# Performance work log

Hardware: AMD Instinct MI355X
Metric: run time of the kernel (lower is better)

Reference implementation:

```python
import jax, jax.numpy as jnp
import numpy as np

B, S, H = 2, 4096, 2048
NH, NKV, D = 16, 4, 128
BS, LOCAL, GLOB, STRIDE = 64, 8, 4, 16
SEL = GLOB + LOCAL
SCALE = D ** -0.5
NEG = -1e9


def rotate_half(x):
    x1, x2 = x[..., : D // 2], x[..., D // 2 :]
    return jnp.concatenate([-x2, x1], axis=-1)


def setup_inputs():
    key = jax.random.key(0)
    ks = jax.random.split(key, 5)
    hidden_states = jax.random.normal(ks[0], (B, S, H), dtype=jnp.float32)
    # standard RoPE tables, shape [B, S, D] as the module expects (cos.unsqueeze(1))
    pos = jnp.arange(S, dtype=jnp.float32)
    inv = 1.0 / (10000.0 ** (jnp.arange(0, D, 2, dtype=jnp.float32) / D))
    freqs = pos[:, None] * inv[None, :]
    emb = jnp.concatenate([freqs, freqs], axis=-1)
    cos = jnp.broadcast_to(jnp.cos(emb)[None], (B, S, D)).astype(jnp.float32)
    sin = jnp.broadcast_to(jnp.sin(emb)[None], (B, S, D)).astype(jnp.float32)
    std = 0.02
    Wq = jax.random.normal(ks[1], (NH * D, H), dtype=jnp.float32) * std
    Wk = jax.random.normal(ks[2], (NKV * D, H), dtype=jnp.float32) * std
    Wv = jax.random.normal(ks[3], (NKV * D, H), dtype=jnp.float32) * std
    Wo = jax.random.normal(ks[4], (H, NH * D), dtype=jnp.float32) * std
    return {"hidden_states": hidden_states, "cos": cos, "sin": sin,
            "Wq": Wq, "Wk": Wk, "Wv": Wv, "Wo": Wo}


def _block_sparse_attn(q, k, v):
    # q, k, v: [B, NH, S, D]; past_len = 0, attention_mask = None (all keys valid)
    qb = S // BS
    kb = S // BS
    qid = jnp.arange(qb)
    # local blocks: the LOCAL most recent blocks ending at the query block
    loc = qid[:, None] - (LOCAL - 1 - jnp.arange(LOCAL)[None, :])
    loc = jnp.clip(loc, 0, kb - 1)
    # global blocks: strided anchors
    g = jnp.clip(jnp.arange(GLOB) * STRIDE, 0, kb - 1)
    glob = jnp.broadcast_to(g[None, :], (qb, GLOB))
    sel = jnp.concatenate([glob, loc], axis=1)  # [qb, SEL]
    valid = sel <= qid[:, None]                 # causal at block level
    # dedup: drop a selected block if an earlier slot selected the same block
    eq = sel[:, :, None] == sel[:, None, :]
    lower = jnp.tril(jnp.ones((SEL, SEL), dtype=bool), k=-1)
    keep = (~(eq & lower[None]).any(-1)) & valid  # [qb, SEL]

    k_blk = k.reshape(B, NH, kb, BS, D)
    v_blk = v.reshape(B, NH, kb, BS, D)
    k_sel = jnp.take(k_blk, sel.reshape(-1), axis=2).reshape(B, NH, qb, SEL * BS, D)
    v_sel = jnp.take(v_blk, sel.reshape(-1), axis=2).reshape(B, NH, qb, SEL * BS, D)
    q_blk = q.reshape(B, NH, qb, BS, D)

    scores = jnp.einsum("bhqid,bhqjd->bhqij", q_blk, k_sel) * SCALE  # [B,NH,qb,BS,SEL*BS]
    keep_tok = jnp.broadcast_to(keep[:, :, None], (qb, SEL, BS)).reshape(qb, SEL * BS)
    scores = scores + (1.0 - keep_tok.astype(scores.dtype))[None, None, :, None, :] * NEG
    # intra-block causal mask where selected block == query block
    same = (sel == qid[:, None]).astype(scores.dtype)  # [qb, SEL]
    intra = jnp.triu(jnp.full((BS, BS), NEG, dtype=scores.dtype), k=1)
    scores6 = scores.reshape(B, NH, qb, BS, SEL, BS)
    scores6 = scores6 + intra[None, None, None, :, None, :] * same[None, None, :, None, :, None]
    scores = scores6.reshape(B, NH, qb, BS, SEL * BS)
    probs = jax.nn.softmax(scores, axis=-1)
    out = jnp.einsum("bhqij,bhqjd->bhqid", probs, v_sel)
    return out.reshape(B, NH, S, D)


def reference(hidden_states, cos, sin, Wq, Wk, Wv, Wo):
    q = (hidden_states @ Wq.T).reshape(B, S, NH, D).transpose(0, 2, 1, 3)
    k = (hidden_states @ Wk.T).reshape(B, S, NKV, D).transpose(0, 2, 1, 3)
    v = (hidden_states @ Wv.T).reshape(B, S, NKV, D).transpose(0, 2, 1, 3)
    c = cos[:, None, :, :]
    s = sin[:, None, :, :]
    q = q * c + rotate_half(q) * s
    k = k * c + rotate_half(k) * s
    rep = NH // NKV
    k = jnp.repeat(k, rep, axis=1)
    v = jnp.repeat(v, rep, axis=1)
    out = _block_sparse_attn(q, k, v)
    out = out.transpose(0, 2, 1, 3).reshape(B, S, NH * D)
    return out @ Wo.T
```

## Files before the change

### kernel.cpp

```cpp
#include <hip/hip_runtime.h>

typedef __bf16 bf16_t;
typedef __bf16 bf16x8_t __attribute__((ext_vector_type(8)));
typedef __bf16 bf16x4_t __attribute__((ext_vector_type(4)));
typedef float f32x4_t __attribute__((ext_vector_type(4)));
typedef unsigned short u16;
typedef unsigned int u32;

#define B_ 2
#define S_ 4096
#define NH_ 16
#define NKV_ 4
#define D_ 128
#define NEG_ (-1000000000.0f)
#define SCALE_ 0.08838834764831845f

__device__ __forceinline__ void load16(const bf16_t* g, bf16_t* l) {
  __builtin_amdgcn_global_load_lds(
      (__attribute__((address_space(1))) void*)(g),
      (__attribute__((address_space(3))) void*)(l),
      16, 0, 0);
}

__global__ __launch_bounds__(256) void cvt_all_kernel(const float* __restrict__ hs,
                                                      const float* __restrict__ Wq,
                                                      const float* __restrict__ Wk,
                                                      const float* __restrict__ Wv,
                                                      const float* __restrict__ Wo,
                                                      bf16_t* __restrict__ Xb,
                                                      bf16_t* __restrict__ Wb,
                                                      bf16_t* __restrict__ Wob) {
  int i = blockIdx.x * 256 + threadIdx.x;
  const float* src; bf16_t* dst; int local;
  if (i < 4194304)      { src = hs; dst = Xb;            local = i; }
  else if (i < 5242880) { src = Wq; dst = Wb;            local = i - 4194304; }
  else if (i < 5505024) { src = Wk; dst = Wb + 4194304;  local = i - 5242880; }
  else if (i < 5767168) { src = Wv; dst = Wb + 5242880;  local = i - 5505024; }
  else                  { src = Wo; dst = Wob;           local = i - 5767168; }
  float4 v = ((const float4*)src)[local];
  bf16x4_t o;
  o.x = (bf16_t)v.x; o.y = (bf16_t)v.y; o.z = (bf16_t)v.z; o.w = (bf16_t)v.w;
  *(bf16x4_t*)(dst + (size_t)local * 4) = o;
}

#define DRAIN2() asm volatile("s_waitcnt vmcnt(2)" ::: "memory")
#define DRAIN4() asm volatile("s_waitcnt vmcnt(4)" ::: "memory")
#define BARF() { __builtin_amdgcn_s_barrier(); asm volatile("" ::: "memory"); }


#define QLDA_(BUF) { \
  _Pragma("unroll") for (int mi = 0; mi < 4; mi++) { \
    _Pragma("unroll") for (int ks = 0; ks < 2; ks++) { \
      a[mi][ks] = *(const bf16x8_t*)&As[BUF][ks][wr4 * 64 + mi * 16 + l15][(l4 ^ xr) * 8]; } } }

#define QLDB_(BUF, NP) { \
  _Pragma("unroll") for (int n2 = 0; n2 < 2; n2++) { \
    _Pragma("unroll") for (int ks = 0; ks < 2; ks++) { \
      b[(NP) * 2 + n2][ks] = *(const bf16x8_t*)&Bs[BUF][ks][wc2 * 64 + ((NP) * 2 + n2) * 16 + l15][(l4 ^ xr) * 8]; } } }

#define QMFMA_(NP) { \
  __builtin_amdgcn_s_setprio(1); \
  _Pragma("unroll") for (int mi = 0; mi < 4; mi++) { \
    _Pragma("unroll") for (int n2 = 0; n2 < 2; n2++) { \
      _Pragma("unroll") for (int ks = 0; ks < 2; ks++) { \
        acc[mi][(NP) * 2 + n2] = __builtin_amdgcn_mfma_f32_16x16x32_bf16( \
            a[mi][ks], b[(NP) * 2 + n2][ks], acc[mi][(NP) * 2 + n2], 0, 0, 0); } } } \
  __builtin_amdgcn_s_setprio(0); }

__global__ __launch_bounds__(512, 2) void gemm_qkv_kernel(const bf16_t* __restrict__ A,
                                                          const bf16_t* __restrict__ Bm,
                                                          bf16_t* __restrict__ Cb,
                                                          int M, int N, int K) {
  __shared__ __align__(16) bf16_t As[2][2][256][32];
  __shared__ __align__(16) bf16_t Bs[2][2][128][32];
  const int t = threadIdx.x;
  const int lane = t & 63;
  const int w = t >> 6;
  const int wr4 = w >> 1;
  const int wc2 = w & 1;
  const int l15 = lane & 15, l4 = lane >> 4;
  const int xr = (l15 >> 1) & 3;
  const int sp = w >> 2;
  const int swi = w & 3;
  const int srow = lane >> 2;
  const int sg = lane & 3;
  const int scg = (srow >> 1) & 3;

  const int m0 = blockIdx.x * 256;
  const int n0 = blockIdx.y * 128;
  const bf16_t* Ablk = A + (size_t)m0 * K;
  const bf16_t* Bblk = Bm + (size_t)n0 * K;

  f32x4_t acc[4][4] = {};
  bf16x8_t a[4][2], b[4][2];

  const int nkt = K >> 6;
  const int nit = nkt >> 1;

  auto stageA = [&](int buf, int mp, int kt) {
#pragma unroll
    for (int c = 0; c < 2; c++) {
      int r0 = c * 128 + mp * 64;
      load16(Ablk + (size_t)(r0 + swi * 16 + srow) * K + kt * 64 + sp * 32 + (sg ^ scg) * 8,
             &As[buf][0][0][0] + buf * 0 + sp * 8192 + (r0 + swi * 16) * 32);
    }
  };
  auto stageB = [&](int buf, int kt) {
#pragma unroll
    for (int c = 0; c < 2; c++) {
      int r0 = c * 64 + swi * 16;
      load16(Bblk + (size_t)(r0 + srow) * K + kt * 64 + sp * 32 + (sg ^ scg) * 8,
             &Bs[buf][0][0][0] + sp * 4096 + r0 * 32);
    }
  };

  stageA(0, 0, 0); stageA(0, 1, 0); stageB(0, 0);
  stageA(1, 0, 1);

#pragma unroll 1
  for (int i = 0; i < nit; i++) {
    const int ktA = 2 * i + 1;
    const int ktB = (2 * i + 2 < nkt) ? 2 * i + 2 : nkt - 1;
    const int ktC = (2 * i + 3 < nkt) ? 2 * i + 3 : nkt - 1;
    DRAIN2(); BARF();
    QLDA_(0); QLDB_(0, 0);
    stageA(1, 1, ktA); stageB(1, ktA);
    QMFMA_(0);
    BARF();
    QLDB_(0, 1);
    stageA(0, 0, ktB);
    QMFMA_(1);
    DRAIN2(); BARF();
    QLDA_(1); QLDB_(1, 0);
    stageA(0, 1, ktB); stageB(0, ktB);
    QMFMA_(0);
    BARF();
    QLDB_(1, 1);
    stageA(1, 0, ktC);
    QMFMA_(1);
  }
  asm volatile("s_waitcnt vmcnt(0)" ::: "memory");

#pragma unroll
  for (int mi = 0; mi < 4; mi++)
#pragma unroll
    for (int ni = 0; ni < 4; ni++)
#pragma unroll
      for (int r = 0; r < 4; r++) {
        int grow = m0 + wr4 * 64 + mi * 16 + l4 * 4 + r;
        int gcol = n0 + wc2 * 64 + ni * 16 + l15;
        Cb[(size_t)grow * N + gcol] = (bf16_t)acc[mi][ni][r];
      }
}

#define LDA_(BUF, MP) { \
  _Pragma("unroll") for (int mi = 0; mi < 4; mi++) { \
    _Pragma("unroll") for (int ks = 0; ks < 2; ks++) { \
      a[mi][ks] = *(const bf16x8_t*)&As[BUF][ks][wr * 128 + (MP) * 64 + mi * 16 + l15][(l4 ^ xr) * 8]; } } }

#define LDB_(BUF, NP) { \
  _Pragma("unroll") for (int n2 = 0; n2 < 2; n2++) { \
    _Pragma("unroll") for (int ks = 0; ks < 2; ks++) { \
      b[(NP) * 2 + n2][ks] = *(const bf16x8_t*)&Bs[BUF][ks][wc * 64 + (NP) * 32 + n2 * 16 + l15][(l4 ^ xr) * 8]; } } }

#define MFMA_Q(MP, NP) { \
  __builtin_amdgcn_s_setprio(1); \
  _Pragma("unroll") for (int mi = 0; mi < 4; mi++) { \
    _Pragma("unroll") for (int n2 = 0; n2 < 2; n2++) { \
      _Pragma("unroll") for (int ks = 0; ks < 2; ks++) { \
        acc[(MP) * 4 + mi][(NP) * 2 + n2] = __builtin_amdgcn_mfma_f32_16x16x32_bf16( \
            a[mi][ks], b[(NP) * 2 + n2][ks], acc[(MP) * 4 + mi][(NP) * 2 + n2], 0, 0, 0); } } } \
  __builtin_amdgcn_s_setprio(0); }

__global__ __launch_bounds__(512, 2) void gemm256_kernel(const bf16_t* __restrict__ A,
                                                         const bf16_t* __restrict__ Bm,
                                                         float* __restrict__ Cf,
                                                         int M, int N, int K) {
  __shared__ __align__(16) bf16_t As[2][2][256][32];
  __shared__ __align__(16) bf16_t Bs[2][2][256][32];
  const int t = threadIdx.x;
  const int lane = t & 63;
  const int w = t >> 6;
  const int wr = w >> 2;
  const int wc = w & 3;
  const int l15 = lane & 15, l4 = lane >> 4;
  const int xr = (l15 >> 1) & 3;
  const int sp = w >> 2;
  const int swi = w & 3;
  const int srow = lane >> 2;
  const int sg = lane & 3;
  const int scg = (srow >> 1) & 3;

  const int m0 = blockIdx.x * 256;
  const int n0 = blockIdx.y * 256;
  const bf16_t* Ablk = A + (size_t)m0 * K;
  const bf16_t* Bblk = Bm + (size_t)n0 * K;

  f32x4_t acc[8][4] = {};
  bf16x8_t a[4][2], b[4][2];

  const int nkt = K >> 6;
  const int nit = nkt >> 1;

  auto stageA = [&](int buf, int mp, int kt) {
#pragma unroll
    for (int c = 0; c < 2; c++) {
      int r0 = c * 128 + mp * 64;
      load16(Ablk + (size_t)(r0 + swi * 16 + srow) * K + kt * 64 + sp * 32 + (sg ^ scg) * 8,
             &As[buf][0][0][0] + sp * 8192 + (r0 + swi * 16) * 32);
    }
  };
  auto stageB = [&](int buf, int np, int kt) {
#pragma unroll
    for (int c = 0; c < 2; c++) {
      int r0 = (c * 2 + (swi >> 1)) * 64 + np * 32 + (swi & 1) * 16;
      load16(Bblk + (size_t)(r0 + srow) * K + kt * 64 + sp * 32 + (sg ^ scg) * 8,
             &Bs[buf][0][0][0] + sp * 8192 + r0 * 32);
    }
  };

  stageA(0, 0, 0); stageB(0, 0, 0); stageA(0, 1, 0); stageB(0, 1, 0);
  stageA(1, 0, 1); stageB(1, 0, 1);

#pragma unroll 1
  for (int i = 0; i < nit; i++) {
    const int ktA = 2 * i + 1;
    const int ktB = (2 * i + 2 < nkt) ? 2 * i + 2 : nkt - 1;
    const int ktC = (2 * i + 3 < nkt) ? 2 * i + 3 : nkt - 1;
    DRAIN4(); BARF();
    LDA_(0, 0); LDB_(0, 0); LDB_(0, 1);
    stageA(1, 1, ktA); stageB(1, 1, ktA);
    MFMA_Q(0, 0); MFMA_Q(0, 1);
    BARF();
    LDA_(0, 1);
    stageB(0, 1, ktB); stageB(0, 0, ktB);
    MFMA_Q(1, 0); MFMA_Q(1, 1);
    DRAIN4(); BARF();
    LDA_(1, 0); LDB_(1, 0); LDB_(1, 1);
    stageA(0, 1, ktB); stageA(0, 0, ktB);
    MFMA_Q(0, 0); MFMA_Q(0, 1);
    BARF();
    LDA_(1, 1);
    stageA(1, 0, ktC); stageB(1, 0, ktC);
    MFMA_Q(1, 0); MFMA_Q(1, 1);
  }
  asm volatile("s_waitcnt vmcnt(0)" ::: "memory");

#pragma unroll
  for (int ar = 0; ar < 8; ar++)
#pragma unroll
    for (int ni = 0; ni < 4; ni++)
#pragma unroll
      for (int r = 0; r < 4; r++) {
        int grow = m0 + wr * 128 + (ar >> 2) * 64 + (ar & 3) * 16 + l4 * 4 + r;
        int gcol = n0 + wc * 64 + ni * 16 + l15;
        Cf[(size_t)grow * N + gcol] = acc[ar][ni][r];
      }
}

__global__ __launch_bounds__(320) void rope_kernel(const bf16_t* __restrict__ qkv,
                                                   const float* __restrict__ cosp,
                                                   const float* __restrict__ sinp,
                                                   bf16_t* __restrict__ Qro,
                                                   bf16_t* __restrict__ Kro) {
  const int tk = blockIdx.x;
  const int b = tk >> 12;
  const int s = tk & 4095;
  const int sblock = s >> 6, row = s & 63;
  const int idx = threadIdx.x;
  int head, lc;
  const bf16_t* base;
  bf16_t* outp;
  if (idx < 256) {
    head = idx >> 4; lc = idx & 15;
    base = qkv + (size_t)tk * 3072 + head * 128;
    outp = Qro + ((size_t)(b * NH_ + head) * 64 + sblock) * 8192;
  } else {
    int i2 = idx - 256;
    head = i2 >> 4; lc = i2 & 15;
    base = qkv + (size_t)tk * 3072 + 2048 + head * 128;
    outp = Kro + ((size_t)(b * NKV_ + head) * 64 + sblock) * 8192;
  }
  const int d0 = lc * 8;
  bf16x8_t x = *(const bf16x8_t*)(base + d0);
  const int d0p = (d0 < 64) ? d0 + 64 : d0 - 64;
  bf16x8_t xp = *(const bf16x8_t*)(base + d0p);
  const float sgn = (d0 < 64) ? -1.0f : 1.0f;
  const float* cb = cosp + (size_t)tk * 128 + d0;
  const float* sb = sinp + (size_t)tk * 128 + d0;
  bf16x8_t o;
#pragma unroll
  for (int e = 0; e < 8; e++)
    o[e] = (bf16_t)((float)x[e] * cb[e] + sgn * (float)xp[e] * sb[e]);
  *(bf16x8_t*)(outp + (lc * 64 + row) * 8) = o;
}

__global__ __launch_bounds__(256) void vtrans_kernel(const u16* __restrict__ qkv,
                                                     u16* __restrict__ vt) {
  __shared__ u16 tile[64][136];
  const int sblock = blockIdx.x;
  const int kh = blockIdx.y;
  const int b = blockIdx.z;
  const int t = threadIdx.x;
#pragma unroll
  for (int i = 0; i < 4; i++) {
    int f = t + 256 * i;
    int sl = f >> 4, c = f & 15;
    uint4 vv = *(const uint4*)(qkv + (size_t)(b * S_ + sblock * 64 + sl) * 3072 + 2560 + kh * 128 + c * 8);
    *(uint4*)&tile[sl][c * 8] = vv;
  }
  __syncthreads();
  u16* out = vt + ((size_t)(b * NKV_ + kh) * 64 + sblock) * 8192;
#pragma unroll
  for (int i = 0; i < 4; i++) {
    int g = t + 256 * i;
    int sc = g >> 7, d = g & 127;
    u16 e0 = tile[sc * 8 + 0][d], e1 = tile[sc * 8 + 1][d];
    u16 e2 = tile[sc * 8 + 2][d], e3 = tile[sc * 8 + 3][d];
    u16 e4 = tile[sc * 8 + 4][d], e5 = tile[sc * 8 + 5][d];
    u16 e6 = tile[sc * 8 + 6][d], e7 = tile[sc * 8 + 7][d];
    uint4 ov;
    ov.x = (u32)e0 | ((u32)e1 << 16);
    ov.y = (u32)e2 | ((u32)e3 << 16);
    ov.z = (u32)e4 | ((u32)e5 << 16);
    ov.w = (u32)e6 | ((u32)e7 << 16);
    *(uint4*)(out + (size_t)g * 8) = ov;
  }
}

__global__ __launch_bounds__(256) void attn_kernel(const bf16_t* __restrict__ Qr,
                                                   const bf16_t* __restrict__ Kr,
                                                   const bf16_t* __restrict__ Vt,
                                                   bf16_t* __restrict__ Ao) {
  __shared__ bf16_t Ks[2][8192];
  __shared__ bf16_t Vs[2][8192];
  __shared__ bf16_t Ps[4 * 16 * 72];
  const int qid = blockIdx.x;
  const int kh = blockIdx.y >> 1;
  const int hp = blockIdx.y & 1;
  const int b = blockIdx.z;
  const int t = threadIdx.x;
  const int lane = t & 63;
  const int w = t >> 6;
  const int l15 = lane & 15, l4 = lane >> 4;
  const int h = kh * 4 + hp * 2 + (w >> 1);
  int row0[2];
  row0[0] = ((w * 2) & 3) * 16;
  row0[1] = ((w * 2 + 1) & 3) * 16;

  int list[12];
  int nkeep = 0;
#pragma unroll
  for (int j = 0; j < 12; j++) {
    int cj;
    if (j < 4) cj = j * 16;
    else { cj = qid - 11 + j; cj = cj < 0 ? 0 : cj; cj = cj > 63 ? 63 : cj; }
    bool keep = (cj <= qid);
#pragma unroll
    for (int i = 0; i < j; i++) {
      int ci;
      if (i < 4) ci = i * 16;
      else { ci = qid - 11 + i; ci = ci < 0 ? 0 : ci; ci = ci > 63 ? 63 : ci; }
      if (ci == cj) keep = false;
    }
    if (keep) list[nkeep++] = cj;
  }

  const bf16_t* Qg = Qr + ((size_t)(b * NH_ + h) * 64 + qid) * 8192;
  const bf16_t* Kg = Kr + ((size_t)(b * NKV_ + kh) * 64) * 8192;
  const bf16_t* Vg = Vt + ((size_t)(b * NKV_ + kh) * 64) * 8192;

  bf16x8_t qa[2][4];
#pragma unroll
  for (int mt = 0; mt < 2; mt++)
#pragma unroll
    for (int ks = 0; ks < 4; ks++)
      qa[mt][ks] = *(const bf16x8_t*)(Qg + ((ks * 4 + l4) * 64 + row0[mt] + l15) * 8);

  bf16x8_t ones;
#pragma unroll
  for (int e = 0; e < 8; e++) ones[e] = (bf16_t)1.0f;

  float mi_r[2][4], li_r[2][4];
  f32x4_t oacc[2][8] = {};
#pragma unroll
  for (int mt = 0; mt < 2; mt++)
#pragma unroll
    for (int r = 0; r < 4; r++) { mi_r[mt][r] = -__builtin_inff(); li_r[mt][r] = 0.0f; }

  {
    int cj = list[0];
#pragma unroll
    for (int i = 0; i < 4; i++) {
      int f = t + 256 * i;
      load16(Kg + (size_t)cj * 8192 + (size_t)f * 8, Ks[0] + (w * 64 + i * 256) * 8);
      load16(Vg + (size_t)cj * 8192 + (size_t)f * 8, Vs[0] + (w * 64 + i * 256) * 8);
    }
  }

  int cur = 0;
#pragma unroll 1
  for (int idx = 0; idx < nkeep; idx++) {
    const int cj = list[idx];
    __syncthreads();
    if (idx + 1 < nkeep) {
      int cn = list[idx + 1];
#pragma unroll
      for (int i = 0; i < 4; i++) {
        int f = t + 256 * i;
        load16(Kg + (size_t)cn * 8192 + (size_t)f * 8, Ks[cur ^ 1] + (w * 64 + i * 256) * 8);
        load16(Vg + (size_t)cn * 8192 + (size_t)f * 8, Vs[cur ^ 1] + (w * 64 + i * 256) * 8);
      }
    }
    const bf16_t* ks_ = Ks[cur];
    const bf16_t* vs_ = Vs[cur];

    f32x4_t sacc[2][4] = {};
#pragma unroll
    for (int ks = 0; ks < 4; ks++)
#pragma unroll
      for (int ni = 0; ni < 4; ni++) {
        bf16x8_t kb = *(const bf16x8_t*)&ks_[((ks * 4 + l4) * 64 + ni * 16 + l15) * 8];
#pragma unroll
        for (int mt = 0; mt < 2; mt++)
          sacc[mt][ni] = __builtin_amdgcn_mfma_f32_16x16x32_bf16(qa[mt][ks], kb, sacc[mt][ni], 0, 0, 0);
      }

    const bool diag = (cj == qid);
    float alpha[2][4];
#pragma unroll
    for (int mt = 0; mt < 2; mt++) {
      float sv[4][4];
#pragma unroll
      for (int ni = 0; ni < 4; ni++)
#pragma unroll
        for (int r = 0; r < 4; r++) {
          float x = sacc[mt][ni][r] * SCALE_;
          if (diag && (ni * 16 + l15) > (row0[mt] + l4 * 4 + r)) x += NEG_;
          sv[ni][r] = x;
        }

      float rmax[4];
#pragma unroll
      for (int r = 0; r < 4; r++)
        rmax[r] = fmaxf(fmaxf(sv[0][r], sv[1][r]), fmaxf(sv[2][r], sv[3][r]));
#pragma unroll
      for (int msk = 1; msk < 16; msk <<= 1)
#pragma unroll
        for (int r = 0; r < 4; r++)
          rmax[r] = fmaxf(rmax[r], __shfl_xor(rmax[r], msk, 64));
#pragma unroll
      for (int r = 0; r < 4; r++) {
        float nm = fmaxf(mi_r[mt][r], rmax[r]);
        alpha[mt][r] = __expf(mi_r[mt][r] - nm);
        mi_r[mt][r] = nm;
      }
      float p[4][4];
#pragma unroll
      for (int ni = 0; ni < 4; ni++)
#pragma unroll
        for (int r = 0; r < 4; r++)
          p[ni][r] = __expf(sv[ni][r] - mi_r[mt][r]);
#pragma unroll
      for (int ni = 0; ni < 4; ni++)
#pragma unroll
        for (int r = 0; r < 4; r++)
          Ps[w * 1152 + (l4 * 4 + r) * 72 + ni * 16 + l15] = (bf16_t)p[ni][r];
#pragma unroll
      for (int n2 = 0; n2 < 8; n2++)
#pragma unroll
        for (int r = 0; r < 4; r++)
          oacc[mt][n2][r] *= alpha[mt][r];

      f32x4_t lacc = {};
#pragma unroll
      for (int kst = 0; kst < 2; kst++) {
        bf16x8_t pa = *(const bf16x8_t*)&Ps[w * 1152 + l15 * 72 + kst * 32 + l4 * 8];
        lacc = __builtin_amdgcn_mfma_f32_16x16x32_bf16(pa, ones, lacc, 0, 0, 0);
#pragma unroll
        for (int n2 = 0; n2 < 8; n2++) {
          bf16x8_t vb = *(const bf16x8_t*)&vs_[((kst * 4 + l4) * 128 + n2 * 16 + l15) * 8];
          oacc[mt][n2] = __builtin_amdgcn_mfma_f32_16x16x32_bf16(pa, vb, oacc[mt][n2], 0, 0, 0);
        }
      }
#pragma unroll
      for (int r = 0; r < 4; r++)
        li_r[mt][r] = li_r[mt][r] * alpha[mt][r] + lacc[r];
    }

    cur ^= 1;
  }

#pragma unroll
  for (int mt = 0; mt < 2; mt++) {
    float invl[4];
#pragma unroll
    for (int r = 0; r < 4; r++) invl[r] = 1.0f / li_r[mt][r];
#pragma unroll
    for (int n2 = 0; n2 < 8; n2++)
#pragma unroll
      for (int r = 0; r < 4; r++) {
        int m = row0[mt] + l4 * 4 + r;
        size_t idx = ((size_t)(b * S_ + qid * 64 + m)) * (NH_ * D_) + h * D_ + n2 * 16 + l15;
        Ao[idx] = (bf16_t)(oacc[mt][n2][r] * invl[r]);
      }
  }
}

extern "C" void kernel_launch(void* const* d_in, const int* in_sizes, int n_in,
                              void* d_out, int out_size, void* d_ws, size_t ws_size,
                              hipStream_t stream) {
  const float* hs = (const float*)d_in[0];
  const float* cosp = (const float*)d_in[1];
  const float* sinp = (const float*)d_in[2];
  const float* Wq = (const float*)d_in[3];
  const float* Wk = (const float*)d_in[4];
  const float* Wv = (const float*)d_in[5];
  const float* Wo = (const float*)d_in[6];
  float* outp = (float*)d_out;

  char* ws = (char*)d_ws;
  bf16_t* Xb   = (bf16_t*)(ws);
  bf16_t* Wb   = (bf16_t*)(ws + 33554432);
  bf16_t* Wob  = (bf16_t*)(ws + 46137344);
  bf16_t* QKVo = (bf16_t*)(ws + 54525952);
  bf16_t* Qr   = (bf16_t*)(ws + 104857600);
  bf16_t* Kr   = (bf16_t*)(ws + 138412032);
  bf16_t* Vt   = (bf16_t*)(ws + 146800640);
  bf16_t* Ao   = QKVo;

  cvt_all_kernel<<<dim3(26624), dim3(256), 0, stream>>>(hs, Wq, Wk, Wv, Wo, Xb, Wb, Wob);

  gemm_qkv_kernel<<<dim3(32, 24), dim3(512), 0, stream>>>(Xb, Wb, QKVo, 8192, 3072, 2048);
  rope_kernel<<<dim3(8192), dim3(320), 0, stream>>>(QKVo, cosp, sinp, Qr, Kr);
  vtrans_kernel<<<dim3(64, NKV_, B_), dim3(256), 0, stream>>>((const u16*)QKVo, (u16*)Vt);
  attn_kernel<<<dim3(64, NKV_ * 2, B_), dim3(256), 0, stream>>>(Qr, Kr, Vt, Ao);
  gemm256_kernel<<<dim3(32, 8), dim3(512), 0, stream>>>(Ao, Wob, outp, 8192, 2048, 2048);
}
```

Baseline: 493.2 us.

## Fold softmax scale into Q, use exp2 with lazy rescale, merge GQA heads per block

Pre-multiplies Q by scale*log2(e) in the RoPE kernel so attention can use exp2 directly without a per-score multiply. The online softmax now rescales the accumulator only when the running max grows by more than 8, which skips most alpha multiplies. The attention block grows to 512 threads and covers all four query heads that share one KV head, so each K/V block is loaded once instead of twice. The P staging buffer is smaller and written per k-step. Risks include bf16 rounding of the pre-scaled Q, larger unnormalised exponents under the lazy threshold, and higher register pressure at 512 threads.

```diff
diff --git a/kernel.cpp b/kernel.cpp
--- a/kernel.cpp
+++ b/kernel.cpp
@@ -12,8 +12,8 @@
 #define NH_ 16
 #define NKV_ 4
 #define D_ 128
-#define NEG_ (-1000000000.0f)
-#define SCALE_ 0.08838834764831845f
+#define QSCALE_ 0.12751743f
+#define NEG2_ (-1442695040.0f)
 
 __device__ __forceinline__ void load16(const bf16_t* g, bf16_t* l) {
   __builtin_amdgcn_global_load_lds(
@@ -47,7 +47,6 @@
 #define DRAIN4() asm volatile("s_waitcnt vmcnt(4)" ::: "memory")
 #define BARF() { __builtin_amdgcn_s_barrier(); asm volatile("" ::: "memory"); }
 
-
 #define QLDA_(BUF) { \
   _Pragma("unroll") for (int mi = 0; mi < 4; mi++) { \
     _Pragma("unroll") for (int ks = 0; ks < 2; ks++) { \
@@ -102,7 +101,7 @@
     for (int c = 0; c < 2; c++) {
       int r0 = c * 128 + mp * 64;
       load16(Ablk + (size_t)(r0 + swi * 16 + srow) * K + kt * 64 + sp * 32 + (sg ^ scg) * 8,
-             &As[buf][0][0][0] + buf * 0 + sp * 8192 + (r0 + swi * 16) * 32);
+             &As[buf][0][0][0] + sp * 8192 + (r0 + swi * 16) * 32);
     }
   };
   auto stageB = [&](int buf, int kt) {
@@ -271,15 +270,18 @@
   int head, lc;
   const bf16_t* base;
   bf16_t* outp;
+  float qs;
   if (idx < 256) {
     head = idx >> 4; lc = idx & 15;
     base = qkv + (size_t)tk * 3072 + head * 128;
     outp = Qro + ((size_t)(b * NH_ + head) * 64 + sblock) * 8192;
+    qs = QSCALE_;
   } else {
     int i2 = idx - 256;
     head = i2 >> 4; lc = i2 & 15;
     base = qkv + (size_t)tk * 3072 + 2048 + head * 128;
     outp = Kro + ((size_t)(b * NKV_ + head) * 64 + sblock) * 8192;
+    qs = 1.0f;
   }
   const int d0 = lc * 8;
   bf16x8_t x = *(const bf16x8_t*)(base + d0);
@@ -291,7 +293,7 @@
   bf16x8_t o;
 #pragma unroll
   for (int e = 0; e < 8; e++)
-    o[e] = (bf16_t)((float)x[e] * cb[e] + sgn * (float)xp[e] * sb[e]);
+    o[e] = (bf16_t)(((float)x[e] * cb[e] + sgn * (float)xp[e] * sb[e]) * qs);
   *(bf16x8_t*)(outp + (lc * 64 + row) * 8) = o;
 }
 
@@ -328,22 +330,21 @@
   }
 }
 
-__global__ __launch_bounds__(256) void attn_kernel(const bf16_t* __restrict__ Qr,
-                                                   const bf16_t* __restrict__ Kr,
-                                                   const bf16_t* __restrict__ Vt,
-                                                   bf16_t* __restrict__ Ao) {
+__global__ __launch_bounds__(512, 4) void attn_kernel(const bf16_t* __restrict__ Qr,
+                                                      const bf16_t* __restrict__ Kr,
+                                                      const bf16_t* __restrict__ Vt,
+                                                      bf16_t* __restrict__ Ao) {
   __shared__ bf16_t Ks[2][8192];
   __shared__ bf16_t Vs[2][8192];
-  __shared__ bf16_t Ps[4 * 16 * 72];
+  __shared__ bf16_t Ps[8 * 640];
   const int qid = blockIdx.x;
-  const int kh = blockIdx.y >> 1;
-  const int hp = blockIdx.y & 1;
+  const int kh = blockIdx.y;
   const int b = blockIdx.z;
   const int t = threadIdx.x;
   const int lane = t & 63;
   const int w = t >> 6;
   const int l15 = lane & 15, l4 = lane >> 4;
-  const int h = kh * 4 + hp * 2 + (w >> 1);
+  const int h = kh * 4 + (w >> 1);
   int row0[2];
   row0[0] = ((w * 2) & 3) * 16;
   row0[1] = ((w * 2 + 1) & 3) * 16;
@@ -391,10 +392,10 @@
   {
     int cj = list[0];
 #pragma unroll
-    for (int i = 0; i < 4; i++) {
-      int f = t + 256 * i;
-      load16(Kg + (size_t)cj * 8192 + (size_t)f * 8, Ks[0] + (w * 64 + i * 256) * 8);
-      load16(Vg + (size_t)cj * 8192 + (size_t)f * 8, Vs[0] + (w * 64 + i * 256) * 8);
+    for (int i = 0; i < 2; i++) {
+      int f = t + 512 * i;
+      load16(Kg + (size_t)cj * 8192 + (size_t)f * 8, Ks[0] + (w * 64 + i * 512) * 8);
+      load16(Vg + (size_t)cj * 8192 + (size_t)f * 8, Vs[0] + (w * 64 + i * 512) * 8);
     }
   }
 
@@ -406,10 +407,10 @@
     if (idx + 1 < nkeep) {
       int cn = list[idx + 1];
 #pragma unroll
-      for (int i = 0; i < 4; i++) {
-        int f = t + 256 * i;
-        load16(Kg + (size_t)cn * 8192 + (size_t)f * 8, Ks[cur ^ 1] + (w * 64 + i * 256) * 8);
-        load16(Vg + (size_t)cn * 8192 + (size_t)f * 8, Vs[cur ^ 1] + (w * 64 + i * 256) * 8);
+      for (int i = 0; i < 2; i++) {
+        int f = t + 512 * i;
+        load16(Kg + (size_t)cn * 8192 + (size_t)f * 8, Ks[cur ^ 1] + (w * 64 + i * 512) * 8);
+        load16(Vg + (size_t)cn * 8192 + (size_t)f * 8, Vs[cur ^ 1] + (w * 64 + i * 512) * 8);
       }
     }
     const bf16_t* ks_ = Ks[cur];
@@ -427,55 +428,61 @@
       }
 
     const bool diag = (cj == qid);
-    float alpha[2][4];
 #pragma unroll
     for (int mt = 0; mt < 2; mt++) {
-      float sv[4][4];
-#pragma unroll
-      for (int ni = 0; ni < 4; ni++)
-#pragma unroll
-        for (int r = 0; r < 4; r++) {
-          float x = sacc[mt][ni][r] * SCALE_;
-          if (diag && (ni * 16 + l15) > (row0[mt] + l4 * 4 + r)) x += NEG_;
-          sv[ni][r] = x;
-        }
-
+      if (diag) {
+#pragma unroll
+        for (int ni = 0; ni < 4; ni++)
+#pragma unroll
+          for (int r = 0; r < 4; r++)
+            if ((ni * 16 + l15) > (row0[mt] + l4 * 4 + r)) sacc[mt][ni][r] += NEG2_;
+      }
       float rmax[4];
 #pragma unroll
       for (int r = 0; r < 4; r++)
-        rmax[r] = fmaxf(fmaxf(sv[0][r], sv[1][r]), fmaxf(sv[2][r], sv[3][r]));
+        rmax[r] = fmaxf(fmaxf(sacc[mt][0][r], sacc[mt][1][r]),
+                        fmaxf(sacc[mt][2][r], sacc[mt][3][r]));
 #pragma unroll
       for (int msk = 1; msk < 16; msk <<= 1)
 #pragma unroll
         for (int r = 0; r < 4; r++)
           rmax[r] = fmaxf(rmax[r], __shfl_xor(rmax[r], msk, 64));
-#pragma unroll
-      for (int r = 0; r < 4; r++) {
-        float nm = fmaxf(mi_r[mt][r], rmax[r]);
-        alpha[mt][r] = __expf(mi_r[mt][r] - nm);
-        mi_r[mt][r] = nm;
+      bool need = false;
+#pragma unroll
+      for (int r = 0; r < 4; r++) need = need || (rmax[r] > mi_r[mt][r] + 8.0f);
+      if (__any(need)) {
+        float alpha[4];
+#pragma unroll
+        for (int r = 0; r < 4; r++) {
+          float nm = fmaxf(mi_r[mt][r], rmax[r]);
+          alpha[r] = exp2f(mi_r[mt][r] - nm);
+          mi_r[mt][r] = nm;
+        }
+#pragma unroll
+        for (int n2 = 0; n2 < 8; n2++)
+#pragma unroll
+          for (int r = 0; r < 4; r++)
+            oacc[mt][n2][r] *= alpha[r];
+#pragma unroll
+        for (int r = 0; r < 4; r++) li_r[mt][r] *= alpha[r];
       }
       float p[4][4];
 #pragma unroll
       for (int ni = 0; ni < 4; ni++)
 #pragma unroll
         for (int r = 0; r < 4; r++)
-          p[ni][r] = __expf(sv[ni][r] - mi_r[mt][r]);
-#pragma unroll
-      for (int ni = 0; ni < 4; ni++)
-#pragma unroll
-        for (int r = 0; r < 4; r++)
-          Ps[w * 1152 + (l4 * 4 + r) * 72 + ni * 16 + l15] = (bf16_t)p[ni][r];
-#pragma unroll
-      for (int n2 = 0; n2 < 8; n2++)
-#pragma unroll
-        for (int r = 0; r < 4; r++)
-          oacc[mt][n2][r] *= alpha[mt][r];
-
+          p[ni][r] = exp2f(sacc[mt][ni][r] - mi_r[mt][r]);
+
+      bf16_t* psw = &Ps[w * 640];
       f32x4_t lacc = {};
 #pragma unroll
       for (int kst = 0; kst < 2; kst++) {
-        bf16x8_t pa = *(const bf16x8_t*)&Ps[w * 1152 + l15 * 72 + kst * 32 + l4 * 8];
+#pragma unroll
+        for (int n2i = 0; n2i < 2; n2i++)
+#pragma unroll
+          for (int r = 0; r < 4; r++)
+            psw[(l4 * 4 + r) * 40 + n2i * 16 + l15] = (bf16_t)p[kst * 2 + n2i][r];
+        bf16x8_t pa = *(const bf16x8_t*)&psw[l15 * 40 + l4 * 8];
         lacc = __builtin_amdgcn_mfma_f32_16x16x32_bf16(pa, ones, lacc, 0, 0, 0);
 #pragma unroll
         for (int n2 = 0; n2 < 8; n2++) {
@@ -485,7 +492,7 @@
       }
 #pragma unroll
       for (int r = 0; r < 4; r++)
-        li_r[mt][r] = li_r[mt][r] * alpha[mt][r] + lacc[r];
+        li_r[mt][r] += lacc[r];
     }
 
     cur ^= 1;
@@ -534,6 +541,6 @@
   gemm_qkv_kernel<<<dim3(32, 24), dim3(512), 0, stream>>>(Xb, Wb, QKVo, 8192, 3072, 2048);
   rope_kernel<<<dim3(8192), dim3(320), 0, stream>>>(QKVo, cosp, sinp, Qr, Kr);
   vtrans_kernel<<<dim3(64, NKV_, B_), dim3(256), 0, stream>>>((const u16*)QKVo, (u16*)Vt);
-  attn_kernel<<<dim3(64, NKV_ * 2, B_), dim3(256), 0, stream>>>(Qr, Kr, Vt, Ao);
+  attn_kernel<<<dim3(64, NKV_, B_), dim3(512), 0, stream>>>(Qr, Kr, Vt, Ao);
   gemm256_kernel<<<dim3(32, 8), dim3(512), 0, stream>>>(Ao, Wob, outp, 8192, 2048, 2048);
 }
```

New measurement: 708.9 us. 1.44x slower.
